# Optimization experiments

Hardware: AMD Instinct MI355X
Metric: run time of the kernel (lower is better)

Reference implementation:

```python
import jax, jax.numpy as jnp
import numpy as np

B, L, C, O, K, KN, A = 32, 4096, 256, 256, 3, 4, 16
BN_EPS = 1e-5


def setup_inputs() -> dict:
    key = jax.random.key(0)
    ks = jax.random.split(key, 12)
    x = jax.random.normal(ks[0], (B, L, C), dtype=jnp.float32)
    # ODConv weight bank [kernel_num, out, in//groups, k], kaiming-ish scale
    weight = jax.random.normal(ks[1], (KN, O, C, K), dtype=jnp.float32) * np.sqrt(2.0 / (O * K))
    w_fc = jax.random.normal(ks[2], (A, C), dtype=jnp.float32) * np.sqrt(2.0 / A)
    bn_gamma = jnp.ones((A,), jnp.float32)
    bn_beta = jnp.zeros((A,), jnp.float32)
    bn_mean = jnp.zeros((A,), jnp.float32)
    bn_var = jnp.ones((A,), jnp.float32)
    w_ch = jax.random.normal(ks[3], (C, A), dtype=jnp.float32) * np.sqrt(2.0 / C)
    b_ch = jnp.zeros((C,), jnp.float32)
    w_fil = jax.random.normal(ks[4], (O, A), dtype=jnp.float32) * np.sqrt(2.0 / O)
    b_fil = jnp.zeros((O,), jnp.float32)
    w_sp = jax.random.normal(ks[5], (K, A), dtype=jnp.float32) * np.sqrt(2.0 / K)
    b_sp = jnp.zeros((K,), jnp.float32)
    w_ker = jax.random.normal(ks[6], (KN, A), dtype=jnp.float32) * np.sqrt(2.0 / KN)
    b_ker = jnp.zeros((KN,), jnp.float32)
    return {"x": x, "weight": weight, "w_fc": w_fc, "bn_gamma": bn_gamma,
            "bn_beta": bn_beta, "bn_mean": bn_mean, "bn_var": bn_var,
            "w_ch": w_ch, "b_ch": b_ch, "w_fil": w_fil, "b_fil": b_fil,
            "w_sp": w_sp, "b_sp": b_sp, "w_ker": w_ker, "b_ker": b_ker}


def reference(x, weight, w_fc, bn_gamma, bn_beta, bn_mean, bn_var,
              w_ch, b_ch, w_fil, b_fil, w_sp, b_sp, w_ker, b_ker):
    # x: [B, L, C] channels-last; attention head uses global-avg-pooled features
    pooled = x.mean(axis=1)                                   # [B, C]
    h = pooled @ w_fc.T                                       # [B, A] (1x1 conv, no bias)
    h = (h - bn_mean) * jax.lax.rsqrt(bn_var + BN_EPS) * bn_gamma + bn_beta
    h = jax.nn.relu(h)
    # temperature = 1.0
    ch_att = jax.nn.sigmoid(h @ w_ch.T + b_ch)                # [B, C]  channel attention
    fil_att = jax.nn.sigmoid(h @ w_fil.T + b_fil)             # [B, O]  filter attention
    sp_att = jax.nn.sigmoid(h @ w_sp.T + b_sp)                # [B, K]  spatial attention
    ker_att = jax.nn.softmax(h @ w_ker.T + b_ker, axis=1)     # [B, KN] kernel attention
    # aggregate per-sample dynamic kernel: [B, O, C, K]
    agg_w = jnp.einsum('bk,bn,noik->boik', sp_att, ker_att, weight)
    xs = x.transpose(0, 2, 1) * ch_att[:, :, None]            # [B, C, L]

    def conv1(xi, wi):  # xi: [C, L], wi: [O, C, K]
        return jax.lax.conv_general_dilated(
            xi[None], wi, window_strides=(1,), padding=[(1, 1)],
            rhs_dilation=(1,), dimension_numbers=('NCH', 'OIH', 'NCH'))[0]

    out = jax.vmap(conv1)(xs, agg_w)                          # [B, O, L]
    return out * fil_att[:, :, None]
```

## Files before the change

### kernel.cpp

```cpp
#include <hip/hip_runtime.h>
#include <hip/hip_bf16.h>
#include <stdint.h>

#define B_ 32
#define L_ 4096
#define C_ 256
#define O_ 256
#define K_ 3
#define KN_ 4
#define A_ 16
#define LP_ 4098

typedef unsigned short u16;
typedef __attribute__((ext_vector_type(8))) short bf16x8;
typedef __attribute__((ext_vector_type(4))) float f32x4;

static __device__ __forceinline__ u16 f2bf(float f) {
    union { float f; uint32_t u; } v; v.f = f;
    uint32_t u = v.u;
    u += 0x7fffu + ((u >> 16) & 1u);
    return (u16)(u >> 16);
}

__global__ __launch_bounds__(256) void poolcvt_k(const float* __restrict__ x,
                                                 u16* __restrict__ xb,
                                                 float* __restrict__ part) {
    __shared__ float red[4][256];
    int bid = blockIdx.x;
    int b = bid >> 5, chunk = bid & 31;
    int t = threadIdx.x;
    int w = t >> 6, lane = t & 63;
    int c0 = lane << 2;
    f32x4 s = {0.f, 0.f, 0.f, 0.f};
    const float* xp = x + ((size_t)b * L_ + (size_t)chunk * 128) * C_ + c0;
    u16* xbb = xb + ((size_t)b * LP_ + (size_t)chunk * 128 + 1) * 256;
    #pragma unroll 4
    for (int it = 0; it < 32; ++it) {
        int rl = it * 4 + w;
        float4 v = *reinterpret_cast<const float4*>(xp + (size_t)rl * C_);
        s.x += v.x; s.y += v.y; s.z += v.z; s.w += v.w;
        ushort4 hv;
        hv.x = f2bf(v.x); hv.y = f2bf(v.y); hv.z = f2bf(v.z); hv.w = f2bf(v.w);
        *reinterpret_cast<ushort4*>(xbb + (size_t)rl * 256 + c0) = hv;
    }
    *reinterpret_cast<f32x4*>(&red[w][c0]) = s;
    __syncthreads();
    part[((size_t)bid << 8) + t] = red[0][t] + red[1][t] + red[2][t] + red[3][t];
    if (chunk == 0 && t < 64)
        *reinterpret_cast<ushort4*>(xb + (size_t)b * LP_ * 256 + t * 4) = make_ushort4(0, 0, 0, 0);
    if (chunk == 31 && t < 64)
        *reinterpret_cast<ushort4*>(xb + ((size_t)b * LP_ + LP_ - 1) * 256 + t * 4) = make_ushort4(0, 0, 0, 0);
}

__global__ __launch_bounds__(256) void pool_partial_k(const float* __restrict__ x,
                                                      float* __restrict__ part) {
    int bid = blockIdx.x;
    int b = bid >> 5, ch = bid & 31;
    int c = threadIdx.x;
    const float* p = x + (size_t)(b * L_ + ch * 128) * C_ + c;
    float s = 0.f;
    #pragma unroll 4
    for (int l = 0; l < 128; ++l) s += p[(size_t)l * C_];
    part[((size_t)bid << 8) + c] = s;
}

__global__ __launch_bounds__(256) void att_k(const float* __restrict__ part,
    const float* __restrict__ w_fc, const float* __restrict__ bn_g,
    const float* __restrict__ bn_b, const float* __restrict__ bn_m,
    const float* __restrict__ bn_v,
    const float* __restrict__ w_ch, const float* __restrict__ b_ch,
    const float* __restrict__ w_fil, const float* __restrict__ b_fil,
    const float* __restrict__ w_sp, const float* __restrict__ b_sp,
    const float* __restrict__ w_ker, const float* __restrict__ b_ker,
    float* __restrict__ ch_att, float* __restrict__ fil_att,
    float* __restrict__ sp_att, float* __restrict__ ker_att) {
    __shared__ float pooled[C_];
    __shared__ float h[A_];
    int b = blockIdx.x, t = threadIdx.x;
    float s = 0.f;
    for (int j = 0; j < 32; ++j) s += part[(((size_t)(b * 32 + j)) << 8) + t];
    pooled[t] = s * (1.0f / L_);
    __syncthreads();
    if (t < A_) {
        float acc = 0.f;
        for (int c = 0; c < C_; ++c) acc += pooled[c] * w_fc[t * C_ + c];
        float sc = bn_g[t] * rsqrtf(bn_v[t] + 1e-5f);
        acc = (acc - bn_m[t]) * sc + bn_b[t];
        h[t] = fmaxf(acc, 0.f);
    }
    __syncthreads();
    {
        float a1 = b_ch[t], a2 = b_fil[t];
        for (int a = 0; a < A_; ++a) { a1 += h[a] * w_ch[t * A_ + a]; a2 += h[a] * w_fil[t * A_ + a]; }
        ch_att[b * C_ + t]  = 1.f / (1.f + expf(-a1));
        fil_att[b * O_ + t] = 1.f / (1.f + expf(-a2));
    }
    if (t < K_) {
        float acc = b_sp[t];
        for (int a = 0; a < A_; ++a) acc += h[a] * w_sp[t * A_ + a];
        sp_att[b * 4 + t] = 1.f / (1.f + expf(-acc));
    }
    if (t == 0) {
        float lg[KN_], m = -1e30f;
        for (int n = 0; n < KN_; ++n) {
            float acc = b_ker[n];
            for (int a = 0; a < A_; ++a) acc += h[a] * w_ker[n * A_ + a];
            lg[n] = acc; m = fmaxf(m, acc);
        }
        float ss = 0.f;
        for (int n = 0; n < KN_; ++n) { lg[n] = expf(lg[n] - m); ss += lg[n]; }
        for (int n = 0; n < KN_; ++n) ker_att[b * 4 + n] = lg[n] / ss;
    }
}

__global__ __launch_bounds__(256) void wfrag_k(const float* __restrict__ weight,
    const float* __restrict__ ch_att, const float* __restrict__ fil_att,
    const float* __restrict__ sp_att, const float* __restrict__ ker_att,
    u16* __restrict__ wf) {
    __shared__ float wlds[64 * 97];
    int beta = blockIdx.x;
    int ob = beta & 15, ic = (beta >> 4) & 7, bg = beta >> 7;
    int t = threadIdx.x;
    const size_t blk_base = (size_t)(ob * 16) * 768 + ic * 96;
    #pragma unroll
    for (int j = 0; j < 24; ++j) {
        int ei = t + (j << 8);
        int r = ei / 96, c = ei - r * 96;
        int n = r >> 4, ol = r & 15;
        wlds[r * 97 + c] = weight[((size_t)n * 256 + ol) * 768 + blk_base + c];
    }
    __syncthreads();
    int lane = t & 63, q = t >> 6;
    int o_l = lane & 15, ig = lane >> 4;
    int i0 = ig << 3;
    int o = (ob << 4) + o_l;
    int ig0 = (ic << 5) + i0;
    float wl[4][3][8];
    #pragma unroll
    for (int n = 0; n < 4; ++n) {
        int rb = (n * 16 + o_l) * 97;
        #pragma unroll
        for (int e = 0; e < 8; ++e) {
            int cb = rb + (i0 + e) * 3;
            wl[n][0][e] = wlds[cb];
            wl[n][1][e] = wlds[cb + 1];
            wl[n][2][e] = wlds[cb + 2];
        }
    }
    #pragma unroll
    for (int bi = 0; bi < 2; ++bi) {
        int b = (bg << 3) + (q << 1) + bi;
        float ka0 = ker_att[b * 4 + 0], ka1 = ker_att[b * 4 + 1];
        float ka2 = ker_att[b * 4 + 2], ka3 = ker_att[b * 4 + 3];
        float fil = fil_att[b * O_ + o];
        float ch8[8];
        *reinterpret_cast<float4*>(ch8)     = *reinterpret_cast<const float4*>(ch_att + b * C_ + ig0);
        *reinterpret_cast<float4*>(ch8 + 4) = *reinterpret_cast<const float4*>(ch_att + b * C_ + ig0 + 4);
        #pragma unroll
        for (int tap = 0; tap < 3; ++tap) {
            float fs = fil * sp_att[b * 4 + tap];
            union { u16 h[8]; uint4 v; } pk;
            #pragma unroll
            for (int e = 0; e < 8; ++e) {
                float acc = ka0 * wl[0][tap][e] + ka1 * wl[1][tap][e]
                          + ka2 * wl[2][tap][e] + ka3 * wl[3][tap][e];
                pk.h[e] = f2bf(acc * fs * ch8[e]);
            }
            size_t idx = ((((size_t)(b * 24 + tap * 8 + ic) * 16 + ob) * 64) + lane) << 3;
            *reinterpret_cast<uint4*>(wf + idx) = pk.v;
        }
    }
}

__global__ __launch_bounds__(512, 4) void conv_k(const u16* __restrict__ xb,
    const u16* __restrict__ wf, float* __restrict__ out) {
    __shared__ uint4 lds4[4160];
    char* lp = (char*)lds4;
    int phys = blockIdx.x;
    int logical = ((phys & 7) << 7) + (phys >> 3);
    int b = logical >> 5, lb = logical & 31;
    int l0 = lb << 7;
    int tid = threadIdx.x;
    const u16* xbb = xb + (size_t)b * LP_ * 256;

    #pragma unroll
    for (int it = 0; it < 9; ++it) {
        int id = tid + (it << 9);
        if (id < 4160) {
            int r = id >> 5, g16 = id & 31;
            bf16x8 v = *reinterpret_cast<const bf16x8*>(xbb + ((size_t)(l0 + r) << 8) + g16 * 8);
            *reinterpret_cast<bf16x8*>(lp + r * 512 + ((g16 ^ (r & 7)) << 4)) = v;
        }
    }
    __syncthreads();

    int w = tid >> 6, lane = tid & 63;
    int wr = w & 3, wc = w >> 2;
    int lrow = lane & 15;
    int g = lane >> 4;

    f32x4 acc[4][4] = {};

    for (int kc = 0; kc < 24; ++kc) {
        int t  = kc >> 3;
        int ic = kc & 7;
        bf16x8 af[4], bfr[4];
        const u16* wp = wf + ((((size_t)(b * 24 + kc) * 16 + wr * 4) * 64 + lane) << 3);
        #pragma unroll
        for (int m = 0; m < 4; ++m)
            af[m] = *reinterpret_cast<const bf16x8*>(wp + (m << 9));
        int slotbase = (ic << 2) + g;
        #pragma unroll
        for (int n = 0; n < 4; ++n) {
            int row = wc * 64 + n * 16 + lrow + t;
            int off = row * 512 + ((slotbase ^ (row & 7)) << 4);
            bfr[n] = *reinterpret_cast<const bf16x8*>(lp + off);
        }
        #pragma unroll
        for (int m = 0; m < 4; ++m)
            #pragma unroll
            for (int n = 0; n < 4; ++n)
                acc[m][n] = __builtin_amdgcn_mfma_f32_16x16x32_bf16(af[m], bfr[n], acc[m][n], 0, 0, 0);
    }

    __syncthreads();

    float* ep = (float*)(lp + w * 8192);
    size_t obase = (size_t)b * O_ * L_;
    int lcol = l0 + wc * 64;
    #pragma unroll
    for (int c2 = 0; c2 < 2; ++c2) {
        #pragma unroll
        for (int m2 = 0; m2 < 2; ++m2) {
            int m = c2 * 2 + m2;
            #pragma unroll
            for (int n = 0; n < 4; ++n) {
                int l_loc = n * 16 + lrow;
                int sl = (l_loc >> 2);
                #pragma unroll
                for (int j = 0; j < 4; ++j) {
                    int o_loc = m2 * 16 + g * 4 + j;
                    ep[o_loc * 64 + ((sl ^ o_loc) & 15) * 4 + (l_loc & 3)] = acc[m][n][j];
                }
            }
        }
        #pragma unroll
        for (int og = 0; og < 8; ++og) {
            int o_loc = og * 4 + g;
            int l4 = lrow;
            float4 v = *reinterpret_cast<float4*>(ep + o_loc * 64 + ((l4 ^ o_loc) & 15) * 4);
            int o = wr * 64 + c2 * 32 + o_loc;
            *reinterpret_cast<float4*>(out + obase + (size_t)o * L_ + lcol + l4 * 4) = v;
        }
        if (c2 == 0) __syncthreads();
    }
}

__global__ __launch_bounds__(512, 4) void conv_fb_k(const float* __restrict__ x,
    const u16* __restrict__ wf, float* __restrict__ out) {
    __shared__ uint4 lds4[4160];
    char* lp = (char*)lds4;
    int phys = blockIdx.x;
    int logical = ((phys & 7) << 7) + (phys >> 3);
    int b = logical >> 5, lb = logical & 31;
    int l0 = lb << 7;
    int tid = threadIdx.x;
    const size_t xbase = (size_t)b * L_ * C_;
    #pragma unroll 4
    for (int it = 0; it < 17; ++it) {
        int id = tid + (it << 9);
        if (id < 8320) {
            int r  = id >> 6;
            int i  = (id & 63) << 2;
            int lg = l0 - 1 + r;
            float4 v = make_float4(0.f, 0.f, 0.f, 0.f);
            if (lg >= 0 && lg < L_)
                v = *reinterpret_cast<const float4*>(x + xbase + (size_t)lg * C_ + i);
            ushort4 hv;
            hv.x = f2bf(v.x); hv.y = f2bf(v.y); hv.z = f2bf(v.z); hv.w = f2bf(v.w);
            int slot = (i >> 3) ^ (r & 7);
            int off = r * 512 + slot * 16 + ((i >> 2) & 1) * 8;
            *reinterpret_cast<ushort4*>(lp + off) = hv;
        }
    }
    __syncthreads();
    int w = tid >> 6, lane = tid & 63;
    int wr = w & 3, wc = w >> 2;
    int lrow = lane & 15;
    int g = lane >> 4;
    f32x4 acc[4][4] = {};
    for (int kc = 0; kc < 24; ++kc) {
        int t  = kc >> 3;
        int ic = kc & 7;
        bf16x8 af[4], bfr[4];
        const u16* wp = wf + ((((size_t)(b * 24 + kc) * 16 + wr * 4) * 64 + lane) << 3);
        #pragma unroll
        for (int m = 0; m < 4; ++m)
            af[m] = *reinterpret_cast<const bf16x8*>(wp + (m << 9));
        int slotbase = (ic << 2) + g;
        #pragma unroll
        for (int n = 0; n < 4; ++n) {
            int row = wc * 64 + n * 16 + lrow + t;
            int off = row * 512 + ((slotbase ^ (row & 7)) << 4);
            bfr[n] = *reinterpret_cast<const bf16x8*>(lp + off);
        }
        #pragma unroll
        for (int m = 0; m < 4; ++m)
            #pragma unroll
            for (int n = 0; n < 4; ++n)
                acc[m][n] = __builtin_amdgcn_mfma_f32_16x16x32_bf16(af[m], bfr[n], acc[m][n], 0, 0, 0);
    }
    __syncthreads();
    float* ep = (float*)(lp + w * 8192);
    size_t obase = (size_t)b * O_ * L_;
    int lcol = l0 + wc * 64;
    #pragma unroll
    for (int c2 = 0; c2 < 2; ++c2) {
        #pragma unroll
        for (int m2 = 0; m2 < 2; ++m2) {
            int m = c2 * 2 + m2;
            #pragma unroll
            for (int n = 0; n < 4; ++n) {
                int l_loc = n * 16 + lrow;
                int sl = (l_loc >> 2);
                #pragma unroll
                for (int j = 0; j < 4; ++j) {
                    int o_loc = m2 * 16 + g * 4 + j;
                    ep[o_loc * 64 + ((sl ^ o_loc) & 15) * 4 + (l_loc & 3)] = acc[m][n][j];
                }
            }
        }
        #pragma unroll
        for (int og = 0; og < 8; ++og) {
            int o_loc = og * 4 + g;
            int l4 = lrow;
            float4 v = *reinterpret_cast<float4*>(ep + o_loc * 64 + ((l4 ^ o_loc) & 15) * 4);
            int o = wr * 64 + c2 * 32 + o_loc;
            *reinterpret_cast<float4*>(out + obase + (size_t)o * L_ + lcol + l4 * 4) = v;
        }
        if (c2 == 0) __syncthreads();
    }
}

extern "C" void kernel_launch(void* const* d_in, const int* in_sizes, int n_in,
                              void* d_out, int out_size, void* d_ws, size_t ws_size,
                              hipStream_t stream) {
    const float* x      = (const float*)d_in[0];
    const float* weight = (const float*)d_in[1];
    const float* w_fc   = (const float*)d_in[2];
    const float* bn_g   = (const float*)d_in[3];
    const float* bn_b   = (const float*)d_in[4];
    const float* bn_m   = (const float*)d_in[5];
    const float* bn_v   = (const float*)d_in[6];
    const float* w_ch   = (const float*)d_in[7];
    const float* b_ch   = (const float*)d_in[8];
    const float* w_fil  = (const float*)d_in[9];
    const float* b_fil  = (const float*)d_in[10];
    const float* w_sp   = (const float*)d_in[11];
    const float* b_sp   = (const float*)d_in[12];
    const float* w_ker  = (const float*)d_in[13];
    const float* b_ker  = (const float*)d_in[14];
    float* out = (float*)d_out;
    char*  ws  = (char*)d_ws;

    float* part    = (float*)ws;
    float* ch_att  = (float*)(ws + (1 << 20));
    float* fil_att = ch_att + 32 * 256;
    float* sp_att  = fil_att + 32 * 256;
    float* ker_att = sp_att + 32 * 4;
    u16*   wfrag   = (u16*)(ws + (1 << 20) + 70 * 1024);
    u16*   xbf     = (u16*)(ws + (16u << 20));
    const size_t need = (16u << 20) + (size_t)B_ * LP_ * 512;

    if (ws_size >= need) {
        poolcvt_k<<<1024, 256, 0, stream>>>(x, xbf, part);
        att_k<<<32, 256, 0, stream>>>(part, w_fc, bn_g, bn_b, bn_m, bn_v,
                                      w_ch, b_ch, w_fil, b_fil, w_sp, b_sp, w_ker, b_ker,
                                      ch_att, fil_att, sp_att, ker_att);
        wfrag_k<<<512, 256, 0, stream>>>(weight, ch_att, fil_att, sp_att, ker_att, wfrag);
        conv_k<<<1024, 512, 0, stream>>>(xbf, wfrag, out);
    } else {
        pool_partial_k<<<1024, 256, 0, stream>>>(x, part);
        att_k<<<32, 256, 0, stream>>>(part, w_fc, bn_g, bn_b, bn_m, bn_v,
                                      w_ch, b_ch, w_fil, b_fil, w_sp, b_sp, w_ker, b_ker,
                                      ch_att, fil_att, sp_att, ker_att);
        wfrag_k<<<512, 256, 0, stream>>>(weight, ch_att, fil_att, sp_att, ker_att, wfrag);
        conv_fb_k<<<1024, 512, 0, stream>>>(x, wfrag, out);
    }
}
```

Measured before the change: 120.4 us.

## Halve conv tile to 64 columns and double-buffer MFMA operand loads

```diff
diff --git a/kernel.cpp b/kernel.cpp
--- a/kernel.cpp
+++ b/kernel.cpp
@@ -172,21 +172,21 @@
     }
 }
 
-__global__ __launch_bounds__(512, 4) void conv_k(const u16* __restrict__ xb,
+__global__ __launch_bounds__(256, 2) void conv_k(const u16* __restrict__ xb,
     const u16* __restrict__ wf, float* __restrict__ out) {
-    __shared__ uint4 lds4[4160];
+    __shared__ uint4 lds4[2112];
     char* lp = (char*)lds4;
     int phys = blockIdx.x;
-    int logical = ((phys & 7) << 7) + (phys >> 3);
-    int b = logical >> 5, lb = logical & 31;
-    int l0 = lb << 7;
+    int logical = ((phys & 7) << 8) + (phys >> 3);
+    int b = logical >> 6, lb = logical & 63;
+    int l0 = lb << 6;
     int tid = threadIdx.x;
     const u16* xbb = xb + (size_t)b * LP_ * 256;
 
     #pragma unroll
     for (int it = 0; it < 9; ++it) {
-        int id = tid + (it << 9);
-        if (id < 4160) {
+        int id = tid + (it << 8);
+        if (id < 2112) {
             int r = id >> 5, g16 = id & 31;
             bf16x8 v = *reinterpret_cast<const bf16x8*>(xbb + ((size_t)(l0 + r) << 8) + g16 * 8);
             *reinterpret_cast<bf16x8*>(lp + r * 512 + ((g16 ^ (r & 7)) << 4)) = v;
@@ -195,39 +195,51 @@
     __syncthreads();
 
     int w = tid >> 6, lane = tid & 63;
-    int wr = w & 3, wc = w >> 2;
+    int wr = w;
     int lrow = lane & 15;
     int g = lane >> 4;
 
     f32x4 acc[4][4] = {};
-
-    for (int kc = 0; kc < 24; ++kc) {
-        int t  = kc >> 3;
-        int ic = kc & 7;
-        bf16x8 af[4], bfr[4];
-        const u16* wp = wf + ((((size_t)(b * 24 + kc) * 16 + wr * 4) * 64 + lane) << 3);
-        #pragma unroll
-        for (int m = 0; m < 4; ++m)
-            af[m] = *reinterpret_cast<const bf16x8*>(wp + (m << 9));
-        int slotbase = (ic << 2) + g;
-        #pragma unroll
-        for (int n = 0; n < 4; ++n) {
-            int row = wc * 64 + n * 16 + lrow + t;
-            int off = row * 512 + ((slotbase ^ (row & 7)) << 4);
-            bfr[n] = *reinterpret_cast<const bf16x8*>(lp + off);
-        }
-        #pragma unroll
-        for (int m = 0; m < 4; ++m)
-            #pragma unroll
-            for (int n = 0; n < 4; ++n)
-                acc[m][n] = __builtin_amdgcn_mfma_f32_16x16x32_bf16(af[m], bfr[n], acc[m][n], 0, 0, 0);
-    }
+    const u16* wp0 = wf + ((((size_t)(b * 24) * 16 + wr * 4) * 64 + lane) << 3);
+
+    #define LOAD_AB(AF, BF, kc) do {                                              \
+        const int tap_ = (kc) >> 3, ic_ = (kc) & 7;                               \
+        _Pragma("unroll")                                                         \
+        for (int m = 0; m < 4; ++m)                                               \
+            AF[m] = *reinterpret_cast<const bf16x8*>(wp0 + (size_t)(kc) * 8192 + (m << 9)); \
+        const int sb_ = (ic_ << 2) + g;                                           \
+        _Pragma("unroll")                                                         \
+        for (int n = 0; n < 4; ++n) {                                             \
+            int row_ = n * 16 + lrow + tap_;                                      \
+            BF[n] = *reinterpret_cast<const bf16x8*>(lp + row_ * 512 + ((sb_ ^ (row_ & 7)) << 4)); \
+        }                                                                         \
+    } while (0)
+
+    #define DO_MFMA(AF, BF) do {                                                  \
+        _Pragma("unroll")                                                         \
+        for (int m = 0; m < 4; ++m)                                               \
+            _Pragma("unroll")                                                     \
+            for (int n = 0; n < 4; ++n)                                           \
+                acc[m][n] = __builtin_amdgcn_mfma_f32_16x16x32_bf16(AF[m], BF[n], acc[m][n], 0, 0, 0); \
+    } while (0)
+
+    bf16x8 afA[4], bfA[4], afB[4], bfB[4];
+    LOAD_AB(afA, bfA, 0);
+    LOAD_AB(afB, bfB, 1);
+    #pragma unroll
+    for (int kc2 = 0; kc2 < 12; ++kc2) {
+        DO_MFMA(afA, bfA);
+        if (kc2 < 11) LOAD_AB(afA, bfA, 2 * kc2 + 2);
+        DO_MFMA(afB, bfB);
+        if (kc2 < 11) LOAD_AB(afB, bfB, 2 * kc2 + 3);
+    }
+    #undef LOAD_AB
+    #undef DO_MFMA
 
     __syncthreads();
 
     float* ep = (float*)(lp + w * 8192);
     size_t obase = (size_t)b * O_ * L_;
-    int lcol = l0 + wc * 64;
     #pragma unroll
     for (int c2 = 0; c2 < 2; ++c2) {
         #pragma unroll
@@ -250,7 +262,7 @@
             int l4 = lrow;
             float4 v = *reinterpret_cast<float4*>(ep + o_loc * 64 + ((l4 ^ o_loc) & 15) * 4);
             int o = wr * 64 + c2 * 32 + o_loc;
-            *reinterpret_cast<float4*>(out + obase + (size_t)o * L_ + lcol + l4 * 4) = v;
+            *reinterpret_cast<float4*>(out + obase + (size_t)o * L_ + l0 + l4 * 4) = v;
         }
         if (c2 == 0) __syncthreads();
     }
@@ -378,7 +390,7 @@
                                       w_ch, b_ch, w_fil, b_fil, w_sp, b_sp, w_ker, b_ker,
                                       ch_att, fil_att, sp_att, ker_att);
         wfrag_k<<<512, 256, 0, stream>>>(weight, ch_att, fil_att, sp_att, ker_att, wfrag);
-        conv_k<<<1024, 512, 0, stream>>>(xbf, wfrag, out);
+        conv_k<<<2048, 256, 0, stream>>>(xbf, wfrag, out);
     } else {
         pool_partial_k<<<1024, 256, 0, stream>>>(x, part);
         att_k<<<32, 256, 0, stream>>>(part, w_fc, bn_g, bn_b, bn_m, bn_v,
```

Result: slower. 134.4 us (+11.6%).
